# Kernel optimization log

Hardware: AMD Instinct MI355X
Metric: run time of the kernel (lower is better)

Reference implementation:

```python
import jax, jax.numpy as jnp
import numpy as np

DN = ('NCHW', 'OIHW', 'NCHW')
COMMITMENT_COST = 0.25


def conv(x, w, b=None, stride=1, pad=0, groups=1):
    o = jax.lax.conv_general_dilated(x, w, (stride, stride), [(pad, pad), (pad, pad)],
                                     feature_group_count=groups, dimension_numbers=DN)
    return o if b is None else o + b[None, :, None, None]


def conv_t(x, w, b=None, stride=2, pad=1, groups=1):
    # w is in torch ConvTranspose2d layout: (in_ch, out_ch//groups, kH, kW)
    in_ch, outg, kh, kw = w.shape
    wf = jnp.flip(w, (-2, -1)).reshape(groups, in_ch // groups, outg, kh, kw)
    wf = wf.transpose(0, 2, 1, 3, 4).reshape(groups * outg, in_ch // groups, kh, kw)
    p = kh - 1 - pad
    o = jax.lax.conv_general_dilated(x, wf, (1, 1), [(p, p), (p, p)],
                                     lhs_dilation=(stride, stride),
                                     feature_group_count=groups, dimension_numbers=DN)
    return o if b is None else o + b[None, :, None, None]


def res_stack(x, w1, w2):
    # w1: (L, nrh, nh//2, 3, 3), w2: (L, nh, nrh//2, 1, 1); groups=2, no bias
    for i in range(w1.shape[0]):
        h = conv(jax.nn.relu(x), w1[i], pad=1, groups=2)
        h = conv(jax.nn.relu(h), w2[i], groups=2)
        x = x + h
    return jax.nn.relu(x)


def vq(z, emb, beta):
    # z: (B, C, H, W); emb: (K, C). EMA updates skipped (eval mode).
    zp = jnp.transpose(z, (0, 2, 3, 1))  # BHWC
    C = emb.shape[1]
    flat = zp.reshape(-1, C)
    d = (jnp.sum(flat ** 2, axis=1, keepdims=True)
         + jnp.sum(emb ** 2, axis=1) - 2.0 * flat @ emb.T)
    idx = jnp.argmin(d, axis=1)
    q = emb[idx].reshape(zp.shape)
    loss = beta * jnp.mean((jax.lax.stop_gradient(q) - zp) ** 2)
    q_st = zp + jax.lax.stop_gradient(q - zp)  # straight-through
    avg = jnp.mean(jax.nn.one_hot(idx, emb.shape[0], dtype=z.dtype), axis=0)
    perplexity = jnp.exp(-jnp.sum(avg * jnp.log(avg + 1e-10)))
    return loss, jnp.transpose(q_st, (0, 3, 1, 2)), perplexity


def _forward(x, eb_dw, eb_db, eb_rw, eb_rb, eb_c1w, eb_c1b, eb_c2w, eb_c2b, eb_c3w, eb_c3b,
             eb_rw1, eb_rw2, et_c1w, et_c1b, et_c2w, et_c2b, et_rw1, et_rw2,
             pvt_w, pvt_b, up_w, up_b, pvb_w, pvb_b, emb_t, emb_b,
             db_c1w, db_c1b, db_rw1, db_rw2, db_t1w, db_t1b, db_t2w, db_t2b,
             db_odw, db_odb, db_orw, db_orb):
    NH = eb_c3w.shape[0]
    ED = emb_t.shape[1]
    # --- EncoderBot ---
    xd = conv(x[:, :1], eb_dw, eb_db)      # depth 1x1 -> NH/4
    xr = conv(x[:, 1:], eb_rw, eb_rb)      # rgb 1x1 -> NH/4
    h = jax.nn.relu(jnp.concatenate([xd, xr], axis=1))
    h = jax.nn.relu(conv(h, eb_c1w, eb_c1b, stride=2, pad=1, groups=2))
    h = jax.nn.relu(conv(h, eb_c2w, eb_c2b, stride=2, pad=1, groups=2))
    h = conv(h, eb_c3w, eb_c3b, pad=1, groups=2)
    enc_b = res_stack(h, eb_rw1, eb_rw2)   # (B, NH, H/4, W/4)
    # --- EncoderTop ---
    t = jax.nn.relu(conv(enc_b, et_c1w, et_c1b, stride=2, pad=1, groups=2))
    t = jax.nn.relu(conv(t, et_c2w, et_c2b, pad=1, groups=2))
    enc_t = res_stack(t, et_rw1, et_rw2)   # (B, NH, H/8, W/8)
    # --- top VQ ---
    zt = conv(enc_t, pvt_w, pvt_b, groups=2)
    loss_t, q_t, perp_t = vq(zt, emb_t, COMMITMENT_COST)
    up_t = conv_t(q_t, up_w, up_b, stride=2, pad=1, groups=2)  # (B, ED, H/4, W/4)
    # --- PreVQBot: regroup channels as (enc_b_d, up_t_d, enc_b_rgb, up_t_rgb) ---
    joined = jnp.concatenate([enc_b[:, :NH // 2], up_t[:, :ED // 2],
                              enc_b[:, NH // 2:], up_t[:, ED // 2:]], axis=1)
    zb = conv(joined, pvb_w, pvb_b, groups=2)
    loss_b, q_b, perp_b = vq(zb, emb_b, COMMITMENT_COST)
    # --- DecoderBot: input cat(up_t, q_b), regrouped (t_d, b_d, t_rgb, b_rgb) ---
    dj = jnp.concatenate([up_t[:, :ED // 2], q_b[:, :ED // 2],
                          up_t[:, ED // 2:], q_b[:, ED // 2:]], axis=1)
    y = conv(dj, db_c1w, db_c1b, pad=1, groups=2)
    y = res_stack(y, db_rw1, db_rw2)
    y = jax.nn.relu(conv_t(y, db_t1w, db_t1b, stride=2, pad=1, groups=2))
    y = conv_t(y, db_t2w, db_t2b, stride=2, pad=1, groups=2)  # (B, NH/4, H, W), no relu
    c = y.shape[1]
    out_d = conv(y[:, :c // 2], db_odw, db_odb)
    out_rgb = conv(y[:, c // 2:], db_orw, db_orb)
    recon = jnp.concatenate([out_d, out_rgb], axis=1)  # (B, 4, H, W)
    return loss_b, loss_t, recon, q_t, q_b


def setup_inputs() -> dict:
    key = jax.random.key(0)
    NH, NRH, L, ED, K = 128, 64, 2, 128, 2048
    B, H, W = 8, 256, 256
    ks = iter(jax.random.split(key, 64))
    def w(*shape):
        return jax.random.normal(next(ks), shape, jnp.float32) * 0.05
    return dict(
        x=jax.random.normal(next(ks), (B, 4, H, W), jnp.float32),
        eb_dw=w(NH // 4, 1, 1, 1), eb_db=w(NH // 4),
        eb_rw=w(NH // 4, 3, 1, 1), eb_rb=w(NH // 4),
        eb_c1w=w(NH // 2, NH // 4, 4, 4), eb_c1b=w(NH // 2),
        eb_c2w=w(NH, NH // 4, 4, 4), eb_c2b=w(NH),
        eb_c3w=w(NH, NH // 2, 3, 3), eb_c3b=w(NH),
        eb_rw1=w(L, NRH, NH // 2, 3, 3), eb_rw2=w(L, NH, NRH // 2, 1, 1),
        et_c1w=w(NH, NH // 2, 4, 4), et_c1b=w(NH),
        et_c2w=w(NH, NH // 2, 3, 3), et_c2b=w(NH),
        et_rw1=w(L, NRH, NH // 2, 3, 3), et_rw2=w(L, NH, NRH // 2, 1, 1),
        pvt_w=w(ED, NH // 2, 1, 1), pvt_b=w(ED),
        up_w=w(ED, ED // 2, 4, 4), up_b=w(ED),
        pvb_w=w(ED, (NH + ED) // 2, 1, 1), pvb_b=w(ED),
        emb_t=jax.random.normal(next(ks), (K, ED), jnp.float32),
        emb_b=jax.random.normal(next(ks), (K, ED), jnp.float32),
        db_c1w=w(NH, ED, 3, 3), db_c1b=w(NH),
        db_rw1=w(L, NRH, NH // 2, 3, 3), db_rw2=w(L, NH, NRH // 2, 1, 1),
        db_t1w=w(NH, NH // 4, 4, 4), db_t1b=w(NH // 2),
        db_t2w=w(NH // 2, NH // 8, 4, 4), db_t2b=w(NH // 4),
        db_odw=w(1, NH // 8, 1, 1), db_odb=w(1),
        db_orw=w(3, NH // 8, 1, 1), db_orb=w(3),
    )


def reference(x, eb_dw, eb_db, eb_rw, eb_rb, eb_c1w, eb_c1b, eb_c2w, eb_c2b, eb_c3w, eb_c3b,
              eb_rw1, eb_rw2, et_c1w, et_c1b, et_c2w, et_c2b, et_rw1, et_rw2,
              pvt_w, pvt_b, up_w, up_b, pvb_w, pvb_b, emb_t, emb_b,
              db_c1w, db_c1b, db_rw1, db_rw2, db_t1w, db_t1b, db_t2w, db_t2b,
              db_odw, db_odb, db_orw, db_orb):
    return _forward(x, eb_dw, eb_db, eb_rw, eb_rb, eb_c1w, eb_c1b, eb_c2w, eb_c2b,
                    eb_c3w, eb_c3b, eb_rw1, eb_rw2, et_c1w, et_c1b, et_c2w, et_c2b,
                    et_rw1, et_rw2, pvt_w, pvt_b, up_w, up_b, pvb_w, pvb_b, emb_t, emb_b,
                    db_c1w, db_c1b, db_rw1, db_rw2, db_t1w, db_t1b, db_t2w, db_t2b,
                    db_odw, db_odb, db_orw, db_orb)
```

## Files before the change

kernel.cpp:

```cpp
#include <hip/hip_runtime.h>
#include <cstddef>

#define TPB 256

__device__ __forceinline__ float4 relu4(float4 v) {
    v.x = fmaxf(v.x, 0.0f); v.y = fmaxf(v.y, 0.0f);
    v.z = fmaxf(v.z, 0.0f); v.w = fmaxf(v.w, 0.0f);
    return v;
}

__device__ __forceinline__ const float* pick_src(const float* a, const float* b,
                                                 int n, int g, int l, int HW) {
    return (l < 64) ? a + ((size_t)n * 128 + g * 64 + l) * HW
                    : b + ((size_t)n * 128 + g * 64 + (l - 64)) * HW;
}

template<int W, int ROWS, int OCB, bool RELU_IN, bool SPLIT>
__global__ __launch_bounds__(256) void conv3_kernel(
    const float* __restrict__ in, const float* __restrict__ in2,
    const float* __restrict__ wgt, const float* __restrict__ bias,
    float* __restrict__ out, int Cin, int Cout, int relu_out)
{
    constexpr int J = ROWS * W / 64;
    constexpr int OCT = OCB * 4;
    constexpr int NW = OCB / 4;
    constexpr int ICB = 8;
    constexpr int IN_H = ROWS + 2, IN_W2 = W + 8;
    constexpr int W4 = W / 4;
    __shared__ float s_in[ICB][IN_H][IN_W2];
    __shared__ float s_w[ICB * 9 * OCT];

    const int tid = threadIdx.x;
    const int tx = tid & 63, ty = tid >> 6;
    const int n = blockIdx.z, oc0 = blockIdx.y * OCT, r0 = blockIdx.x * ROWS;
    const int icg = Cin >> 1, ocg = Cout >> 1;
    const int g = oc0 / ocg;

    float acc[OCB][J];
    #pragma unroll
    for (int o = 0; o < OCB; ++o) {
        const float b = bias ? bias[oc0 + ty * OCB + o] : 0.0f;
        #pragma unroll
        for (int j = 0; j < J; ++j) acc[o][j] = b;
    }

    const float* inb = SPLIT ? nullptr
                             : in + ((size_t)n * Cin + (size_t)g * icg) * (W * W);
// ... 37 lines not shown
                    float4 wv[NW];
                    #pragma unroll
                    for (int u = 0; u < NW; ++u)
                        wv[u] = *(const float4*)(swb + kq * OCT + 4 * u);
                    #pragma unroll
                    for (int j = 0; j < J; ++j) {
                        const int p = j * 64 + tx;
                        const int rr = p / W, cc = p - rr * W;
                        const float v = s_in[icl][rr + ky][cc + 3 + kx];
                        #pragma unroll
                        for (int u = 0; u < NW; ++u) {
                            acc[4 * u + 0][j] = fmaf(wv[u].x, v, acc[4 * u + 0][j]);
                            acc[4 * u + 1][j] = fmaf(wv[u].y, v, acc[4 * u + 1][j]);
                            acc[4 * u + 2][j] = fmaf(wv[u].z, v, acc[4 * u + 2][j]);
                            acc[4 * u + 3][j] = fmaf(wv[u].w, v, acc[4 * u + 3][j]);
                        }
                    }
                }
            }
        }
    }

    const int HWo = W * W;
    float* ob = out + ((size_t)n * Cout + oc0 + ty * OCB) * HWo;
    #pragma unroll
    for (int o = 0; o < OCB; ++o) {
        #pragma unroll
        for (int j = 0; j < J; ++j) {
            const int p = j * 64 + tx;
            const int rr = p / W, cc = p - rr * W;
            float r = acc[o][j];
            if (relu_out) r = fmaxf(r, 0.0f);
            ob[(size_t)o * HWo + (size_t)(r0 + rr) * W + cc] = r;
        }
    }
}

template<int W, int ROWS>
__global__ __launch_bounds__(256) void conv4s2_kernel(
    const float* __restrict__ in, const float* __restrict__ wgt,
    const float* __restrict__ bias, float* __restrict__ out,
    int Cin, int Cout, int relu_out)
{
    constexpr int J = ROWS * W / 64;
    constexpr int ICB = 4;
    constexpr int IN_H = 2 * ROWS + 2, IN_W2 = 2 * W + 8;
    constexpr int W24 = W / 2;
    __shared__ float s_in[ICB][IN_H][IN_W2];
    __shared__ float s_w[ICB * 16 * 32];

    const int tid = threadIdx.x;
    const int tx = tid & 63, ty = tid >> 6;
    const int n = blockIdx.z, oc0 = blockIdx.y * 32, r0 = blockIdx.x * ROWS;
    const int icg = Cin >> 1, ocg = Cout >> 1;
    const int g = oc0 / ocg;
    const int Hin = 2 * W;

    float acc[8][J];
    #pragma unroll
    for (int o = 0; o < 8; ++o) {
        const float b = bias ? bias[oc0 + ty * 8 + o] : 0.0f;
        #pragma unroll
        for (int j = 0; j < J; ++j) acc[o][j] = b;
    }

    const float* inb = in + ((size_t)n * Cin + (size_t)g * icg) * (Hin * Hin);
    for (int ic0 = 0; ic0 < icg; ic0 += ICB) {
        __syncthreads();
        for (int i = tid; i < ICB * IN_H * W24; i += 256) {
            const int icl = i / (IN_H * W24);
            const int rem = i - icl * (IN_H * W24);
            const int rr = rem / W24, c4 = rem - rr * W24;
            const int y = 2 * r0 - 1 + rr;
            float4 v = make_float4(0.f, 0.f, 0.f, 0.f);
            if ((unsigned)y < (unsigned)Hin)
                v = *(const float4*)(inb + (size_t)(ic0 + icl) * (Hin * Hin)
                                     + (size_t)y * Hin + 4 * c4);
            *(float4*)&s_in[icl][rr][4 + 4 * c4] = v;
        }
        for (int i = tid; i < ICB * IN_H; i += 256) {
            const int icl = i / IN_H, rr = i - icl * IN_H;
            s_in[icl][rr][3] = 0.0f;
            s_in[icl][rr][2 * W + 4] = 0.0f;
        }
        for (int i = tid; i < ICB * 16 * 32; i += 256) {
            const int ocl = i & 31, rest = i >> 5;
            const int k = rest & 15, icl = rest >> 4;
            s_w[i] = wgt[((size_t)(oc0 + ocl) * icg + (ic0 + icl)) * 16 + k];
        }
        __syncthreads();

        #pragma unroll 1
        for (int icl = 0; icl < ICB; ++icl) {
            const float* swb = s_w + icl * 512 + ty * 8;
            #pragma unroll
            for (int ky = 0; ky < 4; ++ky) {
                #pragma unroll
                for (int kx = 0; kx < 4; ++kx) {
                    const int kq = ky * 4 + kx;
                    const float4 wA = *(const float4*)(swb + kq * 32);
                    const float4 wB = *(const float4*)(swb + kq * 32 + 4);
                    #pragma unroll
                    for (int j = 0; j < J; ++j) {
                        const int p = j * 64 + tx;
                        const int rr = p / W, cc = p - rr * W;
                        const float v = s_in[icl][2 * rr + ky][2 * cc + 3 + kx];
                        acc[0][j] = fmaf(wA.x, v, acc[0][j]);
                        acc[1][j] = fmaf(wA.y, v, acc[1][j]);
                        acc[2][j] = fmaf(wA.z, v, acc[2][j]);
                        acc[3][j] = fmaf(wA.w, v, acc[3][j]);
                        acc[4][j] = fmaf(wB.x, v, acc[4][j]);
                        acc[5][j] = fmaf(wB.y, v, acc[5][j]);
                        acc[6][j] = fmaf(wB.z, v, acc[6][j]);
                        acc[7][j] = fmaf(wB.w, v, acc[7][j]);
                    }
                }
            }
        }
    }

    const int HWo = W * W;
    float* ob = out + ((size_t)n * Cout + oc0 + ty * 8) * HWo;
    #pragma unroll
    for (int o = 0; o < 8; ++o) {
        #pragma unroll
        for (int j = 0; j < J; ++j) {
            const int p = j * 64 + tx;
            const int rr = p / W, cc = p - rr * W;
            float r = acc[o][j];
            if (relu_out) r = fmaxf(r, 0.0f);
            ob[(size_t)o * HWo + (size_t)(r0 + rr) * W + cc] = r;
        }
    }
}

template<int PX, bool RELU_IN, bool ACC, bool RELU_OUT, bool SPLIT>
__global__ __launch_bounds__(256) void conv1_kernel(
    const float* __restrict__ in, const float* __restrict__ in2,
    const float* __restrict__ wgt, const float* __restrict__ bias,
    float* __restrict__ out, int Cin, int Cout, int HW)
{
    constexpr int J = PX / 64;
    constexpr int PX4 = PX / 4;
    constexpr int ICB = 16;
    __shared__ float s_in[ICB][PX];
    __shared__ float s_w[ICB * 32];

    const int tid = threadIdx.x;
    const int tx = tid & 63, ty = tid >> 6;
    const int n = blockIdx.z, oc0 = blockIdx.y * 32, p0 = blockIdx.x * PX;
    const int icg = Cin >> 1, ocg = Cout >> 1;
    const int g = oc0 / ocg;

    float acc[8][J];
    #pragma unroll
    for (int o = 0; o < 8; ++o) {
        const float b = bias ? bias[oc0 + ty * 8 + o] : 0.0f;
        #pragma unroll
        for (int j = 0; j < J; ++j) acc[o][j] = b;
    }

    const float* inb = SPLIT ? nullptr
                             : in + ((size_t)n * Cin + (size_t)g * icg) * HW + p0;
    for (int ic0 = 0; ic0 < icg; ic0 += ICB) {
        __syncthreads();
        for (int i = tid; i < ICB * PX4; i += 256) {
            const int icl = i / PX4, c4 = i - (i / PX4) * PX4;
            const float* src = SPLIT ? pick_src(in, in2, n, g, ic0 + icl, HW) + p0
                                     : inb + (size_t)(ic0 + icl) * HW;
            float4 v = *(const float4*)(src + 4 * c4);
            if (RELU_IN) v = relu4(v);
            *(float4*)&s_in[icl][4 * c4] = v;
        }
        for (int i = tid; i < ICB * 32; i += 256) {
            const int ocl = i & 31, icl = i >> 5;
            s_w[i] = wgt[(size_t)(oc0 + ocl) * icg + ic0 + icl];
        }
        __syncthreads();

        #pragma unroll 4
        for (int icl = 0; icl < ICB; ++icl) {
            const float4 wA = *(const float4*)(s_w + icl * 32 + ty * 8);
            const float4 wB = *(const float4*)(s_w + icl * 32 + ty * 8 + 4);
            #pragma unroll
            for (int j = 0; j < J; ++j) {
                const float v = s_in[icl][j * 64 + tx];
                acc[0][j] = fmaf(wA.x, v, acc[0][j]);
                acc[1][j] = fmaf(wA.y, v, acc[1][j]);
                acc[2][j] = fmaf(wA.z, v, acc[2][j]);
                acc[3][j] = fmaf(wA.w, v, acc[3][j]);
                acc[4][j] = fmaf(wB.x, v, acc[4][j]);
                acc[5][j] = fmaf(wB.y, v, acc[5][j]);
                acc[6][j] = fmaf(wB.z, v, acc[6][j]);
                acc[7][j] = fmaf(wB.w, v, acc[7][j]);
            }
        }
    }

    float* ob = out + ((size_t)n * Cout + oc0 + ty * 8) * HW + p0;
    #pragma unroll
    for (int o = 0; o < 8; ++o) {
        #pragma unroll
        for (int j = 0; j < J; ++j) {
            const size_t idx = (size_t)o * HW + j * 64 + tx;
            float r = acc[o][j];
            if (ACC) r += ob[idx];
            if (RELU_OUT) r = fmaxf(r, 0.0f);
            ob[idx] = r;
        }
    }
}

template<int W, int ROWS, int OCT>
__global__ __launch_bounds__(64 * (OCT / 8)) void convt4_kernel(
    const float* __restrict__ in, const float* __restrict__ wgt,
    const float* __restrict__ bias, float* __restrict__ out,
    int Cin, int Cout, int relu_out)
{
    constexpr int NTHR = 64 * (OCT / 8);
    constexpr int PXT  = ROWS * W / 64;
    constexpr int WP   = W / 64;
    constexpr int ICB  = 8;
    constexpr int RIN  = ((ROWS + 1) >> 1) + 2;
    constexpr int CIN  = W / 2 + 2;
    __shared__ float s_in[ICB][RIN][CIN];
    __shared__ float s_w[ICB * 16 * OCT];

    const int tid = threadIdx.x;
    const int tx = tid & 63, ty = tid >> 6;
    const int n = blockIdx.z;
    const int oc0 = blockIdx.y * OCT;
    const int r0 = blockIdx.x * ROWS;
    const int icg = Cin >> 1, ocg = Cout >> 1;
    const int g = oc0 / ocg, of0 = oc0 - g * ocg;
    const int Hin = W / 2;
    const int iy_lo = (r0 - 2) >> 1;

    float acc[8][PXT];
    #pragma unroll
    for (int o = 0; o < 8; ++o) {
        const float b = bias ? bias[oc0 + ty * 8 + o] : 0.0f;
// ... 305 lines not shown
    const float* db_rw2 = (const float*)d_in[30];
    const float* db_t1w = (const float*)d_in[31];
    const float* db_t1b = (const float*)d_in[32];
    const float* db_t2w = (const float*)d_in[33];
    const float* db_t2b = (const float*)d_in[34];
    const float* db_odw = (const float*)d_in[35];
    const float* db_odb = (const float*)d_in[36];
    const float* db_orw = (const float*)d_in[37];
    const float* db_orb = (const float*)d_in[38];

    float* ws  = (float*)d_ws;
    float* out = (float*)d_out;

    const size_t OFF_H0   = 0;
    const size_t OFF_H1   = 33554432;
    const size_t OFF_H2   = 0;
    const size_t OFF_ENCB = 4194304;
    const size_t OFF_RH   = 8388608;
    const size_t OFF_T1   = 10485760;
    const size_t OFF_T2   = 11534336;
    const size_t OFF_ZT   = 12582912;
    const size_t OFF_UPT  = 13631488;
    const size_t OFF_ZB   = 17825792;
    const size_t OFF_Y    = 22020096;
    const size_t OFF_Y1   = 26214400;
    const size_t OFF_Y2   = 0;
    const size_t OFF_ENT  = 34603008;
    const size_t OFF_ENB  = 34605056;
    const size_t OFF_LPT  = 34607104;
    const size_t OFF_LPB  = 34607232;
    const size_t NEED     = 41943680;
    if (ws_size < NEED * sizeof(float)) return;

    float* o_loss_b = out + 0;
    float* o_loss_t = out + 1;
    float* o_recon  = out + 2;
    float* o_qt     = out + 2 + 8 * 4 * 65536;
    float* o_qb     = o_qt + 8 * 128 * 1024;

    head_kernel<<<8 * 64 * 16384 / TPB, TPB, 0, stream>>>(
        x, eb_dw, eb_db, eb_rw, eb_rb, ws + OFF_H0);
    conv4s2_kernel<128, 2><<<dim3(64, 2, 8), 256, 0, stream>>>(
        ws + OFF_H0, eb_c1w, eb_c1b, ws + OFF_H1, 64, 64, 1);
    conv4s2_kernel<64, 4><<<dim3(16, 4, 8), 256, 0, stream>>>(
        ws + OFF_H1, eb_c2w, eb_c2b, ws + OFF_H2, 64, 128, 1);
    emb_norm_kernel<<<8, TPB, 0, stream>>>(emb_t, ws + OFF_ENT, 2048);
    emb_norm_kernel<<<8, TPB, 0, stream>>>(emb_b, ws + OFF_ENB, 2048);
    conv3_kernel<64, 4, 8, false, false><<<dim3(16, 4, 8), 256, 0, stream>>>(
        ws + OFF_H2, nullptr, eb_c3w, eb_c3b, ws + OFF_ENCB, 128, 128, 0);
    for (int i = 0; i < 2; ++i) {
        conv3_kernel<64, 4, 4, true, false><<<dim3(16, 4, 8), 256, 0, stream>>>(
            ws + OFF_ENCB, nullptr, eb_rw1 + (size_t)i * 64 * 64 * 9, nullptr,
            ws + OFF_RH, 128, 64, 0);
        if (i == 1)
            conv1_kernel<256, true, true, true, false><<<dim3(16, 4, 8), 256, 0, stream>>>(
                ws + OFF_RH, nullptr, eb_rw2 + (size_t)i * 128 * 32, nullptr,
                ws + OFF_ENCB, 64, 128, 4096);
        else
            conv1_kernel<256, true, true, false, false><<<dim3(16, 4, 8), 256, 0, stream>>>(
                ws + OFF_RH, nullptr, eb_rw2 + (size_t)i * 128 * 32, nullptr,
                ws + OFF_ENCB, 64, 128, 4096);
    }

    conv4s2_kernel<32, 4><<<dim3(8, 4, 8), 256, 0, stream>>>(
        ws + OFF_ENCB, et_c1w, et_c1b, ws + OFF_T1, 128, 128, 1);
    conv3_kernel<32, 4, 8, false, false><<<dim3(8, 4, 8), 256, 0, stream>>>(
        ws + OFF_T1, nullptr, et_c2w, et_c2b, ws + OFF_T2, 128, 128, 1);
    for (int i = 0; i < 2; ++i) {
        conv3_kernel<32, 4, 4, true, false><<<dim3(8, 4, 8), 256, 0, stream>>>(
            ws + OFF_T2, nullptr, et_rw1 + (size_t)i * 64 * 64 * 9, nullptr,
            ws + OFF_RH, 128, 64, 0);
        if (i == 1)
            conv1_kernel<128, true, true, true, false><<<dim3(8, 4, 8), 256, 0, stream>>>(
                ws + OFF_RH, nullptr, et_rw2 + (size_t)i * 128 * 32, nullptr,
                ws + OFF_T2, 64, 128, 1024);
        else
            conv1_kernel<128, true, true, false, false><<<dim3(8, 4, 8), 256, 0, stream>>>(
                ws + OFF_RH, nullptr, et_rw2 + (size_t)i * 128 * 32, nullptr,
                ws + OFF_T2, 64, 128, 1024);
    }

    conv1_kernel<128, false, false, false, false><<<dim3(8, 4, 8), 256, 0, stream>>>(
        ws + OFF_T2, nullptr, pvt_w, pvt_b, ws + OFF_ZT, 128, 128, 1024);
    vq_kernel<<<128, 256, 0, stream>>>(ws + OFF_ZT, emb_t, ws + OFF_ENT, o_qt,
                                       ws + OFF_LPT, 1024, 2048);
    loss_finish_kernel<<<1, 256, 0, stream>>>(ws + OFF_LPT, 128,
                                              0.25f / (8192.0f * 128.0f), o_loss_t);

    convt4_kernel<64, 4, 32><<<dim3(16, 4, 8), 256, 0, stream>>>(
        o_qt, up_w, up_b, ws + OFF_UPT, 128, 128, 0);

    conv1_kernel<256, false, false, false, true><<<dim3(16, 4, 8), 256, 0, stream>>>(
        ws + OFF_ENCB, ws + OFF_UPT, pvb_w, pvb_b, ws + OFF_ZB, 256, 128, 4096);
    vq_kernel<<<512, 256, 0, stream>>>(ws + OFF_ZB, emb_b, ws + OFF_ENB, o_qb,
                                       ws + OFF_LPB, 4096, 2048);
    loss_finish_kernel<<<1, 256, 0, stream>>>(ws + OFF_LPB, 512,
                                              0.25f / (32768.0f * 128.0f), o_loss_b);

    conv3_kernel<64, 4, 8, false, true><<<dim3(16, 4, 8), 256, 0, stream>>>(
        ws + OFF_UPT, o_qb, db_c1w, db_c1b, ws + OFF_Y, 256, 128, 0);
    for (int i = 0; i < 2; ++i) {
        conv3_kernel<64, 4, 4, true, false><<<dim3(16, 4, 8), 256, 0, stream>>>(
            ws + OFF_Y, nullptr, db_rw1 + (size_t)i * 64 * 64 * 9, nullptr,
            ws + OFF_RH, 128, 64, 0);
        if (i == 1)
            conv1_kernel<256, true, true, true, false><<<dim3(16, 4, 8), 256, 0, stream>>>(
                ws + OFF_RH, nullptr, db_rw2 + (size_t)i * 128 * 32, nullptr,
                ws + OFF_Y, 64, 128, 4096);
        else
            conv1_kernel<256, true, true, false, false><<<dim3(16, 4, 8), 256, 0, stream>>>(
                ws + OFF_RH, nullptr, db_rw2 + (size_t)i * 128 * 32, nullptr,
                ws + OFF_Y, 64, 128, 4096);
    }
    convt4_kernel<128, 2, 32><<<dim3(64, 2, 8), 256, 0, stream>>>(
        ws + OFF_Y, db_t1w, db_t1b, ws + OFF_Y1, 128, 64, 1);
    convt4_kernel<256, 2, 16><<<dim3(128, 2, 8), 128, 0, stream>>>(
        ws + OFF_Y1, db_t2w, db_t2b, ws + OFF_Y2, 64, 32, 0);
    outconv_kernel<<<8 * 4 * 16384 / TPB, TPB, 0, stream>>>(
        ws + OFF_Y2, db_odw, db_odb, db_orw, db_orb, o_recon);
}
```

Measured before the change: 1.762 ms.

## Add 64-wide 3x3 conv kernel with 8-row tiles and 2x4 register blocking

Adds a specialized 3x3 grouped conv kernel for 64x64 feature maps. Each block covers 8 output rows and each thread computes a 2x4 output patch per channel, reusing a 4x8 input window held in registers. It replaces the 64-wide conv3 launches in the encoder bottom and decoder, halving the grid so that each shared-memory weight and input load feeds more FMAs. The trade-off is more registers per thread and fewer blocks, which may lower occupancy.

After: 1.890 ms. 7.3% more time.

```diff
diff --git a/kernel.cpp b/kernel.cpp
--- a/kernel.cpp
+++ b/kernel.cpp
@@ -13,6 +13,128 @@
                                                  int n, int g, int l, int HW) {
     return (l < 64) ? a + ((size_t)n * 128 + g * 64 + l) * HW
                     : b + ((size_t)n * 128 + g * 64 + (l - 64)) * HW;
+}
+
+template<int OCB, bool RELU_IN, bool SPLIT>
+__global__ __launch_bounds__(256) void conv3w_kernel(
+    const float* __restrict__ in, const float* __restrict__ in2,
+    const float* __restrict__ wgt, const float* __restrict__ bias,
+    float* __restrict__ out, int Cin, int Cout, int relu_out)
+{
+    constexpr int W = 64;
+    constexpr int ROWS = 8;
+    constexpr int OCT = OCB * 4;
+    constexpr int NW = OCB / 4;
+    constexpr int ICB = 8;
+    constexpr int IN_H = ROWS + 2, IN_W2 = W + 8;
+    constexpr int CPR = W / 4;
+    __shared__ float s_in[ICB][IN_H][IN_W2];
+    __shared__ float s_w[ICB * 9 * OCT];
+
+    const int tid = threadIdx.x;
+    const int tx = tid & 63, ty = tid >> 6;
+    const int row2 = tx >> 4;
+    const int cg   = tx & 15;
+    const int n = blockIdx.z, oc0 = blockIdx.y * OCT, r0 = blockIdx.x * ROWS;
+    const int icg = Cin >> 1, ocg = Cout >> 1;
+    const int g = oc0 / ocg;
+
+    float acc[OCB][2][4];
+    #pragma unroll
+    for (int o = 0; o < OCB; ++o) {
+        const float b = bias ? bias[oc0 + ty * OCB + o] : 0.0f;
+        #pragma unroll
+        for (int rr = 0; rr < 2; ++rr)
+            #pragma unroll
+            for (int j = 0; j < 4; ++j) acc[o][rr][j] = b;
+    }
+
+    const float* inb = SPLIT ? nullptr
+                             : in + ((size_t)n * Cin + (size_t)g * icg) * (W * W);
+
+    for (int ic0 = 0; ic0 < icg; ic0 += ICB) {
+        __syncthreads();
+        for (int i = tid; i < ICB * IN_H * CPR; i += 256) {
+            const int icl = i / (IN_H * CPR);
+            const int rem = i - icl * (IN_H * CPR);
+            const int rr = rem / CPR, c4 = rem - rr * CPR;
+            const int y = r0 - 1 + rr;
+            float4 v = make_float4(0.f, 0.f, 0.f, 0.f);
+            if ((unsigned)y < (unsigned)W) {
+                const float* src = SPLIT ? pick_src(in, in2, n, g, ic0 + icl, W * W)
+                                         : inb + (size_t)(ic0 + icl) * (W * W);
+                v = *(const float4*)(src + (size_t)y * W + 4 * c4);
+            }
+            if (RELU_IN) v = relu4(v);
+            *(float2*)&s_in[icl][rr][2 + 4 * c4] = make_float2(v.x, v.y);
+            *(float2*)&s_in[icl][rr][4 + 4 * c4] = make_float2(v.z, v.w);
+        }
+        for (int i = tid; i < ICB * IN_H; i += 256) {
+            const int icl = i / IN_H, rr = i - icl * IN_H;
+            s_in[icl][rr][0] = 0.0f;
+            s_in[icl][rr][1] = 0.0f;
+            s_in[icl][rr][W + 2] = 0.0f;
+            s_in[icl][rr][W + 3] = 0.0f;
+        }
+        for (int i = tid; i < ICB * 9 * OCT; i += 256) {
+            const int ocl = i % OCT, rest = i / OCT;
+            const int k = rest % 9, icl = rest / 9;
+            s_w[i] = wgt[((size_t)(oc0 + ocl) * icg + (ic0 + icl)) * 9 + k];
+        }
+        __syncthreads();
+
+        #pragma unroll 1
+        for (int icl = 0; icl < ICB; ++icl) {
+            float win[4][8];
+            #pragma unroll
+            for (int t = 0; t < 4; ++t) {
+                const float4 A = *(const float4*)&s_in[icl][2 * row2 + t][4 * cg];
+                const float4 B = *(const float4*)&s_in[icl][2 * row2 + t][4 * cg + 4];
+                win[t][0] = A.x; win[t][1] = A.y; win[t][2] = A.z; win[t][3] = A.w;
+                win[t][4] = B.x; win[t][5] = B.y; win[t][6] = B.z; win[t][7] = B.w;
+            }
+            const float* swb = s_w + icl * 9 * OCT + ty * OCB;
+            #pragma unroll
+            for (int ky = 0; ky < 3; ++ky) {
+                #pragma unroll
+                for (int kx = 0; kx < 3; ++kx) {
+                    const int kq = ky * 3 + kx;
+                    float4 wv[NW];
+                    #pragma unroll
+                    for (int u = 0; u < NW; ++u)
+                        wv[u] = *(const float4*)(swb + kq * OCT + 4 * u);
+                    #pragma unroll
+                    for (int rr = 0; rr < 2; ++rr) {
+                        #pragma unroll
+                        for (int j = 0; j < 4; ++j) {
+                            const float v = win[rr + ky][j + kx + 1];
+                            #pragma unroll
+                            for (int u = 0; u < NW; ++u) {
+                                acc[4 * u + 0][rr][j] = fmaf(wv[u].x, v, acc[4 * u + 0][rr][j]);
+                                acc[4 * u + 1][rr][j] = fmaf(wv[u].y, v, acc[4 * u + 1][rr][j]);
+                                acc[4 * u + 2][rr][j] = fmaf(wv[u].z, v, acc[4 * u + 2][rr][j]);
+                                acc[4 * u + 3][rr][j] = fmaf(wv[u].w, v, acc[4 * u + 3][rr][j]);
+                            }
+                        }
+                    }
+                }
+            }
+        }
+    }
+
+    const int HWo = W * W;
+    float* ob = out + ((size_t)n * Cout + oc0 + ty * OCB) * HWo;
+    #pragma unroll
+    for (int o = 0; o < OCB; ++o) {
+        #pragma unroll
+        for (int rr = 0; rr < 2; ++rr) {
+            float4 r4;
+            r4.x = acc[o][rr][0]; r4.y = acc[o][rr][1];
+            r4.z = acc[o][rr][2]; r4.w = acc[o][rr][3];
+            if (relu_out) r4 = relu4(r4);
+            *(float4*)&ob[(size_t)o * HWo + (size_t)(r0 + 2 * row2 + rr) * W + 4 * cg] = r4;
+        }
+    }
 }
 
 template<int W, int ROWS, int OCB, bool RELU_IN, bool SPLIT>
@@ -676,10 +798,10 @@
         ws + OFF_H1, eb_c2w, eb_c2b, ws + OFF_H2, 64, 128, 1);
     emb_norm_kernel<<<8, TPB, 0, stream>>>(emb_t, ws + OFF_ENT, 2048);
     emb_norm_kernel<<<8, TPB, 0, stream>>>(emb_b, ws + OFF_ENB, 2048);
-    conv3_kernel<64, 4, 8, false, false><<<dim3(16, 4, 8), 256, 0, stream>>>(
+    conv3w_kernel<8, false, false><<<dim3(8, 4, 8), 256, 0, stream>>>(
         ws + OFF_H2, nullptr, eb_c3w, eb_c3b, ws + OFF_ENCB, 128, 128, 0);
     for (int i = 0; i < 2; ++i) {
-        conv3_kernel<64, 4, 4, true, false><<<dim3(16, 4, 8), 256, 0, stream>>>(
+        conv3w_kernel<4, true, false><<<dim3(8, 4, 8), 256, 0, stream>>>(
             ws + OFF_ENCB, nullptr, eb_rw1 + (size_t)i * 64 * 64 * 9, nullptr,
             ws + OFF_RH, 128, 64, 0);
         if (i == 1)
@@ -727,10 +849,10 @@
     loss_finish_kernel<<<1, 256, 0, stream>>>(ws + OFF_LPB, 512,
                                               0.25f / (32768.0f * 128.0f), o_loss_b);
 
-    conv3_kernel<64, 4, 8, false, true><<<dim3(16, 4, 8), 256, 0, stream>>>(
+    conv3w_kernel<8, false, true><<<dim3(8, 4, 8), 256, 0, stream>>>(
         ws + OFF_UPT, o_qb, db_c1w, db_c1b, ws + OFF_Y, 256, 128, 0);
     for (int i = 0; i < 2; ++i) {
-        conv3_kernel<64, 4, 4, true, false><<<dim3(16, 4, 8), 256, 0, stream>>>(
+        conv3w_kernel<4, true, false><<<dim3(8, 4, 8), 256, 0, stream>>>(
             ws + OFF_Y, nullptr, db_rw1 + (size_t)i * 64 * 64 * 9, nullptr,
             ws + OFF_RH, 128, 64, 0);
         if (i == 1)
```

## Pre-transpose conv weights and read them from global/L1 in new conv kernels

Applied to the files above, without the earlier changes.

Adds small kernels that transpose 3x3 and 4x4 conv weights into oc-contiguous layouts in scratch memory. New conv3g, conv1g and conv4s2g kernels read these weights straight from global memory instead of staging them in shared memory. They use larger per-thread output-channel tiles (16 per thread for 3x3/1x1) and a de-interleaved even/odd shared layout for the stride-2 conv. Scratch weight buffers are placed in the output tensor region and in reused workspace offsets, which risks aliasing live data and adds extra launches each call.

Measured after the change: 2.856 ms. 62.1% more time.

```diff
diff --git a/kernel.cpp b/kernel.cpp
--- a/kernel.cpp
+++ b/kernel.cpp
@@ -13,6 +13,287 @@
                                                  int n, int g, int l, int HW) {
     return (l < 64) ? a + ((size_t)n * 128 + g * 64 + l) * HW
                     : b + ((size_t)n * 128 + g * 64 + (l - 64)) * HW;
+}
+
+__global__ void conv3wt_kernel(const float* __restrict__ w, float* __restrict__ t,
+                               int Cout, int icg)
+{
+    const int idx = blockIdx.x * TPB + threadIdx.x;
+    const int total = icg * Cout * 12;
+    if (idx >= total) return;
+    const int kk = idx % 12;
+    const int rest = idx / 12;
+    const int oc = rest % Cout, ic = rest / Cout;
+    t[idx] = (kk < 9) ? w[((size_t)oc * icg + ic) * 9 + kk] : 0.0f;
+}
+
+__global__ void conv4wt_kernel(const float* __restrict__ w, float* __restrict__ t,
+                               int Cout, int icg)
+{
+    const int idx = blockIdx.x * TPB + threadIdx.x;
+    const int total = icg * 16 * Cout;
+    if (idx >= total) return;
+    const int oc = idx % Cout;
+    const int rest = idx / Cout;
+    const int k = rest & 15, ic = rest >> 4;
+    t[idx] = w[((size_t)oc * icg + ic) * 16 + k];
+}
+
+template<int GSPAN, bool RELU_IN, bool SPLIT>
+__global__ __launch_bounds__(256) void conv3g_kernel(
+    const float* __restrict__ in, const float* __restrict__ in2,
+    const float* __restrict__ wt, const float* __restrict__ bias,
+    float* __restrict__ out, int Cin, int Cout, int relu_out)
+{
+    constexpr int W = 64;
+    constexpr int ICB = 16;
+    __shared__ float s_in[GSPAN][ICB][3][66];
+
+    const int tid = threadIdx.x;
+    const int tx = tid & 63, ty = tid >> 6;
+    const int n = blockIdx.z, oc0 = blockIdx.y * 64, r0 = blockIdx.x;
+    const int icg = Cin >> 1, ocg = Cout >> 1;
+    const int slot = (GSPAN == 2) ? (ty >> 1) : 0;
+    const int gbase = (GSPAN == 2) ? 0 : (oc0 / ocg);
+
+    float acc[16];
+    #pragma unroll
+    for (int o = 0; o < 16; ++o)
+        acc[o] = bias ? bias[oc0 + ty * 16 + o] : 0.0f;
+
+    for (int ic0 = 0; ic0 < icg; ic0 += ICB) {
+        __syncthreads();
+        for (int i = tid; i < GSPAN * ICB * 3 * 16; i += 256) {
+            const int c4 = i & 15;
+            const int t2 = i >> 4;
+            const int r = t2 % 3;
+            const int t3 = t2 / 3;
+            const int icl = t3 % ICB, s = t3 / ICB;
+            const int y = r0 - 1 + r;
+            const int gs = (GSPAN == 2) ? s : gbase;
+            float4 v = make_float4(0.f, 0.f, 0.f, 0.f);
+            if ((unsigned)y < (unsigned)W) {
+                const float* src = SPLIT ? pick_src(in, in2, n, gs, ic0 + icl, 4096)
+                                         : in + ((size_t)n * Cin + (size_t)gs * icg
+                                                 + ic0 + icl) * 4096;
+                v = *(const float4*)(src + (size_t)y * W + 4 * c4);
+            }
+            if (RELU_IN) v = relu4(v);
+            float* d = &s_in[s][icl][r][1 + 4 * c4];
+            d[0] = v.x; d[1] = v.y; d[2] = v.z; d[3] = v.w;
+        }
+        for (int i = tid; i < GSPAN * ICB * 3; i += 256) {
+            const int r = i % 3;
+            const int t3 = i / 3;
+            const int icl = t3 % ICB, s = t3 / ICB;
+            s_in[s][icl][r][0] = 0.0f;
+            s_in[s][icl][r][65] = 0.0f;
+        }
+        __syncthreads();
+
+        #pragma unroll 1
+        for (int icl = 0; icl < ICB; ++icl) {
+            const int ic = ic0 + icl;
+            float v0 = s_in[slot][icl][0][tx];
+            float v1 = s_in[slot][icl][0][tx + 1];
+            float v2 = s_in[slot][icl][0][tx + 2];
+            float v3 = s_in[slot][icl][1][tx];
+            float v4 = s_in[slot][icl][1][tx + 1];
+            float v5 = s_in[slot][icl][1][tx + 2];
+            float v6 = s_in[slot][icl][2][tx];
+            float v7 = s_in[slot][icl][2][tx + 1];
+            float v8 = s_in[slot][icl][2][tx + 2];
+            #pragma unroll
+            for (int o = 0; o < 16; ++o) {
+                const float* wp = wt + ((size_t)ic * Cout + oc0 + ty * 16 + o) * 12;
+                const float4 wa = *(const float4*)(wp);
+                const float4 wb = *(const float4*)(wp + 4);
+                const float wc = wp[8];
+                float a = acc[o];
+                a = fmaf(wa.x, v0, a);
+                a = fmaf(wa.y, v1, a);
+                a = fmaf(wa.z, v2, a);
+                a = fmaf(wa.w, v3, a);
+                a = fmaf(wb.x, v4, a);
+                a = fmaf(wb.y, v5, a);
+                a = fmaf(wb.z, v6, a);
+                a = fmaf(wb.w, v7, a);
+                a = fmaf(wc, v8, a);
+                acc[o] = a;
+            }
+        }
+    }
+
+    float* ob = out + ((size_t)n * Cout + oc0 + ty * 16) * 4096 + (size_t)r0 * 64 + tx;
+    #pragma unroll
+    for (int o = 0; o < 16; ++o) {
+        float r = acc[o];
+        if (relu_out) r = fmaxf(r, 0.0f);
+        ob[(size_t)o * 4096] = r;
+    }
+}
+
+template<int J, bool RELU_IN, bool ACC, bool RELU_OUT, bool SPLIT>
+__global__ __launch_bounds__(256) void conv1g_kernel(
+    const float* __restrict__ in, const float* __restrict__ in2,
+    const float* __restrict__ wgt, const float* __restrict__ bias,
+    float* __restrict__ out, int Cin, int Cout, int HW)
+{
+    const int tid = threadIdx.x;
+    const int tx = tid & 63, ty = tid >> 6;
+    const int n = blockIdx.z, oc0 = blockIdx.y * 64, p0 = blockIdx.x * 64 * J;
+    const int icg = Cin >> 1, ocg = Cout >> 1;
+    const int g = oc0 / ocg;
+
+    float acc[16][J];
+    #pragma unroll
+    for (int o = 0; o < 16; ++o) {
+        const float b = bias ? bias[oc0 + ty * 16 + o] : 0.0f;
+        #pragma unroll
+        for (int j = 0; j < J; ++j) acc[o][j] = b;
+    }
+
+    #pragma unroll 2
+    for (int ic = 0; ic < icg; ic += 4) {
+        float v[4][J];
+        #pragma unroll
+        for (int q = 0; q < 4; ++q) {
+            const float* src = SPLIT ? pick_src(in, in2, n, g, ic + q, HW)
+                                     : in + ((size_t)n * Cin + (size_t)g * icg
+                                             + ic + q) * HW;
+            #pragma unroll
+            for (int j = 0; j < J; ++j) {
+                float t = src[p0 + j * 64 + tx];
+                if (RELU_IN) t = fmaxf(t, 0.0f);
+                v[q][j] = t;
+            }
+        }
+        #pragma unroll
+        for (int o = 0; o < 16; ++o) {
+            const float4 w = *(const float4*)&wgt[(size_t)(oc0 + ty * 16 + o) * icg + ic];
+            #pragma unroll
+            for (int j = 0; j < J; ++j) {
+                float a = acc[o][j];
+                a = fmaf(w.x, v[0][j], a);
+                a = fmaf(w.y, v[1][j], a);
+                a = fmaf(w.z, v[2][j], a);
+                a = fmaf(w.w, v[3][j], a);
+                acc[o][j] = a;
+            }
+        }
+    }
+
+    float* ob = out + ((size_t)n * Cout + oc0 + ty * 16) * HW + p0;
+    #pragma unroll
+    for (int o = 0; o < 16; ++o) {
+        #pragma unroll
+        for (int j = 0; j < J; ++j) {
+            const size_t idx = (size_t)o * HW + j * 64 + tx;
+            float r = acc[o][j];
+            if (ACC) r += ob[idx];
+            if (RELU_OUT) r = fmaxf(r, 0.0f);
+            ob[idx] = r;
+        }
+    }
+}
+
+template<int W, int ROWS>
+__global__ __launch_bounds__(256) void conv4s2g_kernel(
+    const float* __restrict__ in, const float* __restrict__ wt,
+    const float* __restrict__ bias, float* __restrict__ out,
+    int Cin, int Cout, int relu_out)
+{
+    constexpr int J = ROWS * W / 64;
+    constexpr int ICB = 4;
+    constexpr int IN_H = 2 * ROWS + 2;
+    constexpr int W24 = W / 2;
+    __shared__ float s_e[ICB][IN_H][W + 1];
+    __shared__ float s_o[ICB][IN_H][W + 1];
+
+    const int tid = threadIdx.x;
+    const int tx = tid & 63, ty = tid >> 6;
+    const int n = blockIdx.z, oc0 = blockIdx.y * 32, r0 = blockIdx.x * ROWS;
+    const int icg = Cin >> 1, ocg = Cout >> 1;
+    const int g = oc0 / ocg;
+    const int Hin = 2 * W;
+
+    float acc[8][J];
+    #pragma unroll
+    for (int o = 0; o < 8; ++o) {
+        const float b = bias ? bias[oc0 + ty * 8 + o] : 0.0f;
+        #pragma unroll
+        for (int j = 0; j < J; ++j) acc[o][j] = b;
+    }
+
+    const float* inb = in + ((size_t)n * Cin + (size_t)g * icg) * (Hin * Hin);
+    for (int ic0 = 0; ic0 < icg; ic0 += ICB) {
+        __syncthreads();
+        for (int i = tid; i < ICB * IN_H * W24; i += 256) {
+            const int c4 = i % W24;
+            const int rr = (i / W24) % IN_H;
+            const int icl = i / (W24 * IN_H);
+            const int y = 2 * r0 - 1 + rr;
+            float4 v = make_float4(0.f, 0.f, 0.f, 0.f);
+            if ((unsigned)y < (unsigned)Hin)
+                v = *(const float4*)(inb + (size_t)(ic0 + icl) * (Hin * Hin)
+                                     + (size_t)y * Hin + 4 * c4);
+            s_e[icl][rr][2 * c4]     = v.x;
+            s_o[icl][rr][2 * c4 + 1] = v.y;
+            s_e[icl][rr][2 * c4 + 1] = v.z;
+            s_o[icl][rr][2 * c4 + 2] = v.w;
+        }
+        for (int i = tid; i < ICB * IN_H; i += 256) {
+            const int rr = i % IN_H, icl = i / IN_H;
+            s_o[icl][rr][0] = 0.0f;
+            s_e[icl][rr][W] = 0.0f;
+        }
+        __syncthreads();
+
+        #pragma unroll 1
+        for (int icl = 0; icl < ICB; ++icl) {
+            const int ic = ic0 + icl;
+            #pragma unroll
+            for (int kq = 0; kq < 16; ++kq) {
+                const int ky = kq >> 2, kx = kq & 3;
+                const float* wp = wt + ((size_t)(ic * 16 + kq) * Cout + oc0 + ty * 8);
+                const float4 wA = *(const float4*)(wp);
+                const float4 wB = *(const float4*)(wp + 4);
+                #pragma unroll
+                for (int j = 0; j < J; ++j) {
+                    const int p = j * 64 + tx;
+                    const int rr = p / W, cc = p - rr * W;
+                    const int row = 2 * rr + ky;
+                    float v;
+                    if (kx == 0)      v = s_o[icl][row][cc];
+                    else if (kx == 1) v = s_e[icl][row][cc];
+                    else if (kx == 2) v = s_o[icl][row][cc + 1];
+                    else              v = s_e[icl][row][cc + 1];
+                    acc[0][j] = fmaf(wA.x, v, acc[0][j]);
+                    acc[1][j] = fmaf(wA.y, v, acc[1][j]);
+                    acc[2][j] = fmaf(wA.z, v, acc[2][j]);
+                    acc[3][j] = fmaf(wA.w, v, acc[3][j]);
+                    acc[4][j] = fmaf(wB.x, v, acc[4][j]);
+                    acc[5][j] = fmaf(wB.y, v, acc[5][j]);
+                    acc[6][j] = fmaf(wB.z, v, acc[6][j]);
+                    acc[7][j] = fmaf(wB.w, v, acc[7][j]);
+                }
+            }
+        }
+    }
+
+    const int HWo = W * W;
+    float* ob = out + ((size_t)n * Cout + oc0 + ty * 8) * HWo;
+    #pragma unroll
+    for (int o = 0; o < 8; ++o) {
+        #pragma unroll
+        for (int j = 0; j < J; ++j) {
+            const int p = j * 64 + tx;
+            const int rr = p / W, cc = p - rr * W;
+            float r = acc[o][j];
+            if (relu_out) r = fmaxf(r, 0.0f);
+            ob[(size_t)o * HWo + (size_t)(r0 + rr) * W + cc] = r;
+        }
+    }
 }
 
 template<int W, int ROWS, int OCB, bool RELU_IN, bool SPLIT>
@@ -116,181 +397,6 @@
             float r = acc[o][j];
             if (relu_out) r = fmaxf(r, 0.0f);
             ob[(size_t)o * HWo + (size_t)(r0 + rr) * W + cc] = r;
-        }
-    }
-}
-
-template<int W, int ROWS>
-__global__ __launch_bounds__(256) void conv4s2_kernel(
-    const float* __restrict__ in, const float* __restrict__ wgt,
-    const float* __restrict__ bias, float* __restrict__ out,
-    int Cin, int Cout, int relu_out)
-{
-    constexpr int J = ROWS * W / 64;
-    constexpr int ICB = 4;
-    constexpr int IN_H = 2 * ROWS + 2, IN_W2 = 2 * W + 8;
-    constexpr int W24 = W / 2;
-    __shared__ float s_in[ICB][IN_H][IN_W2];
-    __shared__ float s_w[ICB * 16 * 32];
-
-    const int tid = threadIdx.x;
-    const int tx = tid & 63, ty = tid >> 6;
-    const int n = blockIdx.z, oc0 = blockIdx.y * 32, r0 = blockIdx.x * ROWS;
-    const int icg = Cin >> 1, ocg = Cout >> 1;
-    const int g = oc0 / ocg;
-    const int Hin = 2 * W;
-
-    float acc[8][J];
-    #pragma unroll
-    for (int o = 0; o < 8; ++o) {
-        const float b = bias ? bias[oc0 + ty * 8 + o] : 0.0f;
-        #pragma unroll
-        for (int j = 0; j < J; ++j) acc[o][j] = b;
-    }
-
-    const float* inb = in + ((size_t)n * Cin + (size_t)g * icg) * (Hin * Hin);
-    for (int ic0 = 0; ic0 < icg; ic0 += ICB) {
-        __syncthreads();
-        for (int i = tid; i < ICB * IN_H * W24; i += 256) {
-            const int icl = i / (IN_H * W24);
-            const int rem = i - icl * (IN_H * W24);
-            const int rr = rem / W24, c4 = rem - rr * W24;
-            const int y = 2 * r0 - 1 + rr;
-            float4 v = make_float4(0.f, 0.f, 0.f, 0.f);
-            if ((unsigned)y < (unsigned)Hin)
-                v = *(const float4*)(inb + (size_t)(ic0 + icl) * (Hin * Hin)
-                                     + (size_t)y * Hin + 4 * c4);
-            *(float4*)&s_in[icl][rr][4 + 4 * c4] = v;
-        }
-        for (int i = tid; i < ICB * IN_H; i += 256) {
-            const int icl = i / IN_H, rr = i - icl * IN_H;
-            s_in[icl][rr][3] = 0.0f;
-            s_in[icl][rr][2 * W + 4] = 0.0f;
-        }
-        for (int i = tid; i < ICB * 16 * 32; i += 256) {
-            const int ocl = i & 31, rest = i >> 5;
-            const int k = rest & 15, icl = rest >> 4;
-            s_w[i] = wgt[((size_t)(oc0 + ocl) * icg + (ic0 + icl)) * 16 + k];
-        }
-        __syncthreads();
-
-        #pragma unroll 1
-        for (int icl = 0; icl < ICB; ++icl) {
-            const float* swb = s_w + icl * 512 + ty * 8;
-            #pragma unroll
-            for (int ky = 0; ky < 4; ++ky) {
-                #pragma unroll
-                for (int kx = 0; kx < 4; ++kx) {
-                    const int kq = ky * 4 + kx;
-                    const float4 wA = *(const float4*)(swb + kq * 32);
-                    const float4 wB = *(const float4*)(swb + kq * 32 + 4);
-                    #pragma unroll
-                    for (int j = 0; j < J; ++j) {
-                        const int p = j * 64 + tx;
-                        const int rr = p / W, cc = p - rr * W;
-                        const float v = s_in[icl][2 * rr + ky][2 * cc + 3 + kx];
-                        acc[0][j] = fmaf(wA.x, v, acc[0][j]);
-                        acc[1][j] = fmaf(wA.y, v, acc[1][j]);
-                        acc[2][j] = fmaf(wA.z, v, acc[2][j]);
-                        acc[3][j] = fmaf(wA.w, v, acc[3][j]);
-                        acc[4][j] = fmaf(wB.x, v, acc[4][j]);
-                        acc[5][j] = fmaf(wB.y, v, acc[5][j]);
-                        acc[6][j] = fmaf(wB.z, v, acc[6][j]);
-                        acc[7][j] = fmaf(wB.w, v, acc[7][j]);
-                    }
-                }
-            }
-        }
-    }
-
-    const int HWo = W * W;
-    float* ob = out + ((size_t)n * Cout + oc0 + ty * 8) * HWo;
-    #pragma unroll
-    for (int o = 0; o < 8; ++o) {
-        #pragma unroll
-        for (int j = 0; j < J; ++j) {
-            const int p = j * 64 + tx;
-            const int rr = p / W, cc = p - rr * W;
-            float r = acc[o][j];
-            if (relu_out) r = fmaxf(r, 0.0f);
-            ob[(size_t)o * HWo + (size_t)(r0 + rr) * W + cc] = r;
-        }
-    }
-}
-
-template<int PX, bool RELU_IN, bool ACC, bool RELU_OUT, bool SPLIT>
-__global__ __launch_bounds__(256) void conv1_kernel(
-    const float* __restrict__ in, const float* __restrict__ in2,
-    const float* __restrict__ wgt, const float* __restrict__ bias,
-    float* __restrict__ out, int Cin, int Cout, int HW)
-{
-    constexpr int J = PX / 64;
-    constexpr int PX4 = PX / 4;
-    constexpr int ICB = 16;
-    __shared__ float s_in[ICB][PX];
-    __shared__ float s_w[ICB * 32];
-
-    const int tid = threadIdx.x;
-    const int tx = tid & 63, ty = tid >> 6;
-    const int n = blockIdx.z, oc0 = blockIdx.y * 32, p0 = blockIdx.x * PX;
-    const int icg = Cin >> 1, ocg = Cout >> 1;
-    const int g = oc0 / ocg;
-
-    float acc[8][J];
-    #pragma unroll
-    for (int o = 0; o < 8; ++o) {
-        const float b = bias ? bias[oc0 + ty * 8 + o] : 0.0f;
-        #pragma unroll
-        for (int j = 0; j < J; ++j) acc[o][j] = b;
-    }
-
-    const float* inb = SPLIT ? nullptr
-                             : in + ((size_t)n * Cin + (size_t)g * icg) * HW + p0;
-    for (int ic0 = 0; ic0 < icg; ic0 += ICB) {
-        __syncthreads();
-        for (int i = tid; i < ICB * PX4; i += 256) {
-            const int icl = i / PX4, c4 = i - (i / PX4) * PX4;
-            const float* src = SPLIT ? pick_src(in, in2, n, g, ic0 + icl, HW) + p0
-                                     : inb + (size_t)(ic0 + icl) * HW;
-            float4 v = *(const float4*)(src + 4 * c4);
-            if (RELU_IN) v = relu4(v);
-            *(float4*)&s_in[icl][4 * c4] = v;
-        }
-        for (int i = tid; i < ICB * 32; i += 256) {
-            const int ocl = i & 31, icl = i >> 5;
-            s_w[i] = wgt[(size_t)(oc0 + ocl) * icg + ic0 + icl];
-        }
-        __syncthreads();
-
-        #pragma unroll 4
-        for (int icl = 0; icl < ICB; ++icl) {
-            const float4 wA = *(const float4*)(s_w + icl * 32 + ty * 8);
-            const float4 wB = *(const float4*)(s_w + icl * 32 + ty * 8 + 4);
-            #pragma unroll
-            for (int j = 0; j < J; ++j) {
-                const float v = s_in[icl][j * 64 + tx];
-                acc[0][j] = fmaf(wA.x, v, acc[0][j]);
-                acc[1][j] = fmaf(wA.y, v, acc[1][j]);
-                acc[2][j] = fmaf(wA.z, v, acc[2][j]);
-                acc[3][j] = fmaf(wA.w, v, acc[3][j]);
-                acc[4][j] = fmaf(wB.x, v, acc[4][j]);
-                acc[5][j] = fmaf(wB.y, v, acc[5][j]);
-                acc[6][j] = fmaf(wB.z, v, acc[6][j]);
-                acc[7][j] = fmaf(wB.w, v, acc[7][j]);
-            }
-        }
-    }
-
-    float* ob = out + ((size_t)n * Cout + oc0 + ty * 8) * HW + p0;
-    #pragma unroll
-    for (int o = 0; o < 8; ++o) {
-        #pragma unroll
-        for (int j = 0; j < J; ++j) {
-            const size_t idx = (size_t)o * HW + j * 64 + tx;
-            float r = acc[o][j];
-            if (ACC) r += ob[idx];
-            if (RELU_OUT) r = fmaxf(r, 0.0f);
-            ob[idx] = r;
         }
     }
 }
@@ -662,38 +768,71 @@
     const size_t NEED     = 41943680;
     if (ws_size < NEED * sizeof(float)) return;
 
+    float* WT_EBC1 = out + 4;
+    float* WT_EBC2 = out + 4 + 32768;
+    const size_t WT_EBC3    = 34611200;
+    const size_t WT_DBC1    = 34709504;
+    const size_t WT_RW1_EB0 = 34906112;
+    const size_t WT_RW1_EB1 = 34955264;
+    const size_t WT_RW1_DB0 = 35004416;
+    const size_t WT_RW1_DB1 = 35053568;
+    const size_t WT_ETC1    = 35102720;
+    (void)OFF_Y1;
+
     float* o_loss_b = out + 0;
     float* o_loss_t = out + 1;
     float* o_recon  = out + 2;
     float* o_qt     = out + 2 + 8 * 4 * 65536;
     float* o_qb     = o_qt + 8 * 128 * 1024;
 
+    conv4wt_kernel<<<(32 * 16 * 64 + TPB - 1) / TPB, TPB, 0, stream>>>(
+        eb_c1w, WT_EBC1, 64, 32);
+    conv4wt_kernel<<<(32 * 16 * 128 + TPB - 1) / TPB, TPB, 0, stream>>>(
+        eb_c2w, WT_EBC2, 128, 32);
+
     head_kernel<<<8 * 64 * 16384 / TPB, TPB, 0, stream>>>(
         x, eb_dw, eb_db, eb_rw, eb_rb, ws + OFF_H0);
-    conv4s2_kernel<128, 2><<<dim3(64, 2, 8), 256, 0, stream>>>(
-        ws + OFF_H0, eb_c1w, eb_c1b, ws + OFF_H1, 64, 64, 1);
-    conv4s2_kernel<64, 4><<<dim3(16, 4, 8), 256, 0, stream>>>(
-        ws + OFF_H1, eb_c2w, eb_c2b, ws + OFF_H2, 64, 128, 1);
+    conv4s2g_kernel<128, 2><<<dim3(64, 2, 8), 256, 0, stream>>>(
+        ws + OFF_H0, WT_EBC1, eb_c1b, ws + OFF_H1, 64, 64, 1);
+    conv4s2g_kernel<64, 4><<<dim3(16, 4, 8), 256, 0, stream>>>(
+        ws + OFF_H1, WT_EBC2, eb_c2b, ws + OFF_H2, 64, 128, 1);
+
+    conv3wt_kernel<<<(64 * 128 * 12 + TPB - 1) / TPB, TPB, 0, stream>>>(
+        eb_c3w, ws + WT_EBC3, 128, 64);
+    conv3wt_kernel<<<(128 * 128 * 12 + TPB - 1) / TPB, TPB, 0, stream>>>(
+        db_c1w, ws + WT_DBC1, 128, 128);
+    conv3wt_kernel<<<(64 * 64 * 12 + TPB - 1) / TPB, TPB, 0, stream>>>(
+        eb_rw1, ws + WT_RW1_EB0, 64, 64);
+    conv3wt_kernel<<<(64 * 64 * 12 + TPB - 1) / TPB, TPB, 0, stream>>>(
+        eb_rw1 + 64 * 64 * 9, ws + WT_RW1_EB1, 64, 64);
+    conv3wt_kernel<<<(64 * 64 * 12 + TPB - 1) / TPB, TPB, 0, stream>>>(
+        db_rw1, ws + WT_RW1_DB0, 64, 64);
+    conv3wt_kernel<<<(64 * 64 * 12 + TPB - 1) / TPB, TPB, 0, stream>>>(
+        db_rw1 + 64 * 64 * 9, ws + WT_RW1_DB1, 64, 64);
+    conv4wt_kernel<<<(64 * 16 * 128 + TPB - 1) / TPB, TPB, 0, stream>>>(
+        et_c1w, ws + WT_ETC1, 128, 64);
+
     emb_norm_kernel<<<8, TPB, 0, stream>>>(emb_t, ws + OFF_ENT, 2048);
     emb_norm_kernel<<<8, TPB, 0, stream>>>(emb_b, ws + OFF_ENB, 2048);
-    conv3_kernel<64, 4, 8, false, false><<<dim3(16, 4, 8), 256, 0, stream>>>(
-        ws + OFF_H2, nullptr, eb_c3w, eb_c3b, ws + OFF_ENCB, 128, 128, 0);
+
+    conv3g_kernel<1, false, false><<<dim3(64, 2, 8), 256, 0, stream>>>(
+        ws + OFF_H2, nullptr, ws + WT_EBC3, eb_c3b, ws + OFF_ENCB, 128, 128, 0);
     for (int i = 0; i < 2; ++i) {
-        conv3_kernel<64, 4, 4, true, false><<<dim3(16, 4, 8), 256, 0, stream>>>(
-            ws + OFF_ENCB, nullptr, eb_rw1 + (size_t)i * 64 * 64 * 9, nullptr,
+        conv3g_kernel<2, true, false><<<dim3(64, 1, 8), 256, 0, stream>>>(
+            ws + OFF_ENCB, nullptr, ws + (i ? WT_RW1_EB1 : WT_RW1_EB0), nullptr,
             ws + OFF_RH, 128, 64, 0);
         if (i == 1)
-            conv1_kernel<256, true, true, true, false><<<dim3(16, 4, 8), 256, 0, stream>>>(
+            conv1g_kernel<2, true, true, true, false><<<dim3(32, 2, 8), 256, 0, stream>>>(
                 ws + OFF_RH, nullptr, eb_rw2 + (size_t)i * 128 * 32, nullptr,
                 ws + OFF_ENCB, 64, 128, 4096);
         else
-            conv1_kernel<256, true, true, false, false><<<dim3(16, 4, 8), 256, 0, stream>>>(
+            conv1g_kernel<2, true, true, false, false><<<dim3(32, 2, 8), 256, 0, stream>>>(
                 ws + OFF_RH, nullptr, eb_rw2 + (size_t)i * 128 * 32, nullptr,
                 ws + OFF_ENCB, 64, 128, 4096);
     }
 
-    conv4s2_kernel<32, 4><<<dim3(8, 4, 8), 256, 0, stream>>>(
-        ws + OFF_ENCB, et_c1w, et_c1b, ws + OFF_T1, 128, 128, 1);
+    conv4s2g_kernel<32, 4><<<dim3(8, 4, 8), 256, 0, stream>>>(
+        ws + OFF_ENCB, ws + WT_ETC1, et_c1b, ws + OFF_T1, 128, 128, 1);
     conv3_kernel<32, 4, 8, false, false><<<dim3(8, 4, 8), 256, 0, stream>>>(
         ws + OFF_T1, nullptr, et_c2w, et_c2b, ws + OFF_T2, 128, 128, 1);
     for (int i = 0; i < 2; ++i) {
@@ -701,16 +840,16 @@
             ws + OFF_T2, nullptr, et_rw1 + (size_t)i * 64 * 64 * 9, nullptr,
             ws + OFF_RH, 128, 64, 0);
         if (i == 1)
-            conv1_kernel<128, true, true, true, false><<<dim3(8, 4, 8), 256, 0, stream>>>(
+            conv1g_kernel<1, true, true, true, false><<<dim3(16, 2, 8), 256, 0, stream>>>(
                 ws + OFF_RH, nullptr, et_rw2 + (size_t)i * 128 * 32, nullptr,
                 ws + OFF_T2, 64, 128, 1024);
         else
-            conv1_kernel<128, true, true, false, false><<<dim3(8, 4, 8), 256, 0, stream>>>(
+            conv1g_kernel<1, true, true, false, false><<<dim3(16, 2, 8), 256, 0, stream>>>(
                 ws + OFF_RH, nullptr, et_rw2 + (size_t)i * 128 * 32, nullptr,
                 ws + OFF_T2, 64, 128, 1024);
     }
 
-    conv1_kernel<128, false, false, false, false><<<dim3(8, 4, 8), 256, 0, stream>>>(
+    conv1g_kernel<1, false, false, false, false><<<dim3(16, 2, 8), 256, 0, stream>>>(
         ws + OFF_T2, nullptr, pvt_w, pvt_b, ws + OFF_ZT, 128, 128, 1024);
     vq_kernel<<<128, 256, 0, stream>>>(ws + OFF_ZT, emb_t, ws + OFF_ENT, o_qt,
                                        ws + OFF_LPT, 1024, 2048);
@@ -720,32 +859,32 @@
     convt4_kernel<64, 4, 32><<<dim3(16, 4, 8), 256, 0, stream>>>(
         o_qt, up_w, up_b, ws + OFF_UPT, 128, 128, 0);
 
-    conv1_kernel<256, false, false, false, true><<<dim3(16, 4, 8), 256, 0, stream>>>(
+    conv1g_kernel<2, false, false, false, true><<<dim3(32, 2, 8), 256, 0, stream>>>(
         ws + OFF_ENCB, ws + OFF_UPT, pvb_w, pvb_b, ws + OFF_ZB, 256, 128, 4096);
     vq_kernel<<<512, 256, 0, stream>>>(ws + OFF_ZB, emb_b, ws + OFF_ENB, o_qb,
                                        ws + OFF_LPB, 4096, 2048);
     loss_finish_kernel<<<1, 256, 0, stream>>>(ws + OFF_LPB, 512,
                                               0.25f / (32768.0f * 128.0f), o_loss_b);
 
-    conv3_kernel<64, 4, 8, false, true><<<dim3(16, 4, 8), 256, 0, stream>>>(
-        ws + OFF_UPT, o_qb, db_c1w, db_c1b, ws + OFF_Y, 256, 128, 0);
+    conv3g_kernel<1, false, true><<<dim3(64, 2, 8), 256, 0, stream>>>(
+        ws + OFF_UPT, o_qb, ws + WT_DBC1, db_c1b, ws + OFF_Y, 256, 128, 0);
     for (int i = 0; i < 2; ++i) {
-        conv3_kernel<64, 4, 4, true, false><<<dim3(16, 4, 8), 256, 0, stream>>>(
-            ws + OFF_Y, nullptr, db_rw1 + (size_t)i * 64 * 64 * 9, nullptr,
+        conv3g_kernel<2, true, false><<<dim3(64, 1, 8), 256, 0, stream>>>(
+            ws + OFF_Y, nullptr, ws + (i ? WT_RW1_DB1 : WT_RW1_DB0), nullptr,
             ws + OFF_RH, 128, 64, 0);
         if (i == 1)
-            conv1_kernel<256, true, true, true, false><<<dim3(16, 4, 8), 256, 0, stream>>>(
+            conv1g_kernel<2, true, true, true, false><<<dim3(32, 2, 8), 256, 0, stream>>>(
                 ws + OFF_RH, nullptr, db_rw2 + (size_t)i * 128 * 32, nullptr,
                 ws + OFF_Y, 64, 128, 4096);
         else
-            conv1_kernel<256, true, true, false, false><<<dim3(16, 4, 8), 256, 0, stream>>>(
+            conv1g_kernel<2, true, true, false, false><<<dim3(32, 2, 8), 256, 0, stream>>>(
                 ws + OFF_RH, nullptr, db_rw2 + (size_t)i * 128 * 32, nullptr,
                 ws + OFF_Y, 64, 128, 4096);
     }
     convt4_kernel<128, 2, 32><<<dim3(64, 2, 8), 256, 0, stream>>>(
-        ws + OFF_Y, db_t1w, db_t1b, ws + OFF_Y1, 128, 64, 1);
+        ws + OFF_Y, db_t1w, db_t1b, ws + 26214400, 128, 64, 1);
     convt4_kernel<256, 2, 16><<<dim3(128, 2, 8), 128, 0, stream>>>(
-        ws + OFF_Y1, db_t2w, db_t2b, ws + OFF_Y2, 64, 32, 0);
+        ws + 26214400, db_t2w, db_t2b, ws + OFF_Y2, 64, 32, 0);
     outconv_kernel<<<8 * 4 * 16384 / TPB, TPB, 0, stream>>>(
         ws + OFF_Y2, db_odw, db_odb, db_orw, db_orb, o_recon);
 }
```
